# Kernel tuning notes

Hardware: AMD Instinct MI355X
Metric: run time of the kernel (lower is better)

The kernel has to match this reference:

```python
import jax, jax.numpy as jnp
import numpy as np

# dims: batch, dna_seq_len, protein_emb, decoder_size, ffn hidden, vocab, layers, heads
B, T, P, D, F, V, L, H = 64, 128, 1024, 512, 2048, 4096, 4, 8


def _sinusoid_pe(T, D):
    pos = np.arange(T, dtype=np.float32)[:, None]
    div = np.exp(np.arange(0, D, 2, dtype=np.float32) * (-np.log(10000.0) / D))
    pe = np.zeros((T, D), dtype=np.float32)
    pe[:, 0::2] = np.sin(pos * div)
    pe[:, 1::2] = np.cos(pos * div)
    return jnp.asarray(pe)


def setup_inputs() -> dict:
    key = jax.random.key(0)
    ks = iter(jax.random.split(key, 24))
    n = lambda *shape: jax.random.normal(next(ks), shape, jnp.float32) * 0.02
    return dict(
        protein_embeddings=jax.random.normal(next(ks), (B, P), jnp.float32),
        input_token=jax.random.randint(next(ks), (B,), 0, V),
        proj1_w=n(P, 2 * D), proj1_b=jnp.zeros((2 * D,), jnp.float32),
        proj2_w=n(2 * D, D), proj2_b=jnp.zeros((D,), jnp.float32),
        emb=n(V, D),
        sa_w=n(L, 4, D, D), sa_b=jnp.zeros((L, 4, D), jnp.float32),
        ca_w=n(L, 4, D, D), ca_b=jnp.zeros((L, 4, D), jnp.float32),
        ffn_w1=n(L, D, F), ffn_b1=jnp.zeros((L, F), jnp.float32),
        ffn_w2=n(L, F, D), ffn_b2=jnp.zeros((L, D), jnp.float32),
        ln_g=jnp.ones((L, 3, D), jnp.float32), ln_b=jnp.zeros((L, 3, D), jnp.float32),
        out_w=n(D, V), out_b=jnp.zeros((V,), jnp.float32),
        pe=_sinusoid_pe(T, D),
    )


def _layer_norm(x, g, b, eps=1e-5):
    m = jnp.mean(x, -1, keepdims=True)
    v = jnp.var(x, -1, keepdims=True)
    return (x - m) * jax.lax.rsqrt(v + eps) * g + b


def _forward(protein_embeddings, input_token, proj1_w, proj1_b, proj2_w, proj2_b,
             emb, sa_w, sa_b, ca_w, ca_b, ffn_w1, ffn_b1, ffn_w2, ffn_b2,
             ln_g, ln_b, out_w, out_b, pe):
    dh = D // H
    scale = 1.0 / jnp.sqrt(jnp.float32(dh))
    # protein -> decoder memory: Linear(P, 2D) -> ReLU -> Linear(2D, D),
    # then repeated along seq dim (memory rows are all identical).
    h = jax.nn.relu(protein_embeddings @ proj1_w + proj1_b)
    mem1 = h @ proj2_w + proj2_b                         # [B, D]
    mem = jnp.broadcast_to(mem1[:, None, :], (B, T, D))  # [B, T, D]
    # Cross-attn K/V are constant across decode steps: precompute per layer.
    K = (jnp.einsum('btd,lde->lbte', mem, ca_w[:, 1]) + ca_b[:, 1][:, None, None, :]).reshape(L, B, T, H, dh)
    Vv = (jnp.einsum('btd,lde->lbte', mem, ca_w[:, 2]) + ca_b[:, 2][:, None, None, :]).reshape(L, B, T, H, dh)

    def step(token, t):
        # query length == 1 (the module embeds only the current token each step)
        x = emb[token] + pe[t]                           # [B, D]
        for l in range(L):
            # self-attn over a single key: softmax over one score == 1,
            # so attn output reduces to Wo(Wv x + bv) + bo
            sa = (x @ sa_w[l, 2] + sa_b[l, 2]) @ sa_w[l, 3] + sa_b[l, 3]
            x = _layer_norm(x + sa, ln_g[l, 0], ln_b[l, 0])
            # cross-attention over protein memory
            q = ((x @ ca_w[l, 0] + ca_b[l, 0]) * scale).reshape(B, H, dh)
            s = jnp.einsum('bhe,bthe->bht', q, K[l])
            a = jax.nn.softmax(s, -1)
            o = jnp.einsum('bht,bthe->bhe', a, Vv[l]).reshape(B, D)
            ca = o @ ca_w[l, 3] + ca_b[l, 3]
            x = _layer_norm(x + ca, ln_g[l, 1], ln_b[l, 1])
            # FFN (ReLU, post-LN as in PyTorch default TransformerDecoderLayer)
            f = jax.nn.relu(x @ ffn_w1[l] + ffn_b1[l]) @ ffn_w2[l] + ffn_b2[l]
            x = _layer_norm(x + f, ln_g[l, 2], ln_b[l, 2])
        logits = x @ out_w + out_b                       # [B, V]
        probs = jax.nn.softmax(logits, -1)
        return jnp.argmax(probs, -1), probs

    _, probs_t = jax.lax.scan(step, input_token, jnp.arange(T))
    return jnp.transpose(probs_t, (1, 0, 2))             # [B, T, V]


def reference(protein_embeddings, input_token, proj1_w, proj1_b, proj2_w, proj2_b,
              emb, sa_w, sa_b, ca_w, ca_b, ffn_w1, ffn_b1, ffn_w2, ffn_b2,
              ln_g, ln_b, out_w, out_b, pe):
    return _forward(protein_embeddings, input_token, proj1_w, proj1_b, proj2_w, proj2_b,
                    emb, sa_w, sa_b, ca_w, ca_b, ffn_w1, ffn_b1, ffn_w2, ffn_b2,
                    ln_g, ln_b, out_w, out_b, pe)
```

## Files before the change

kernel.cpp:

```cpp
#include <hip/hip_runtime.h>


#define B 64
#define T 128
#define PP 1024
#define D 512
#define F 2048
#define V 4096
#define XP 20

typedef const float* fp;

static __device__ __forceinline__ float wred(float s){
    #pragma unroll
    for (int o = 32; o > 0; o >>= 1) s += __shfl_xor(s, o, 64);
    return s;
}

__global__ __launch_bounds__(256) void k_setup_mem(
    fp prot, fp p1w, fp p1b, fp p2w, fp p2b,
    fp caw, fp cab, float* ca_out)
{
    __shared__ float xp[PP];
    __shared__ float hr[PP];
    __shared__ float m1[D];
    __shared__ float tv[D];
    int b = blockIdx.x, tid = threadIdx.x;
    for (int i = tid; i < PP; i += 256) xp[i] = prot[b*PP + i];
    __syncthreads();
    for (int c = tid; c < 1024; c += 256){
        float acc = p1b[c];
        for (int k = 0; k < PP; k++) acc = fmaf(xp[k], p1w[k*1024 + c], acc);
        hr[c] = fmaxf(acc, 0.f);
    }
    __syncthreads();
    for (int c = tid; c < D; c += 256){
        float acc = p2b[c];
        for (int k = 0; k < 1024; k++) acc = fmaf(hr[k], p2w[k*D + c], acc);
        m1[c] = acc;
    }
    __syncthreads();
    for (int l = 0; l < 4; l++){
        const float* wv = caw + (size_t)(l*4 + 2)*D*D;
        const float* bv = cab + (l*4 + 2)*D;
        for (int c = tid; c < D; c += 256){
            float acc = bv[c];
            for (int k = 0; k < D; k++) acc = fmaf(m1[k], wv[k*D + c], acc);
            tv[c] = acc;
        }
        __syncthreads();
        const float* wo = caw + (size_t)(l*4 + 3)*D*D;
        const float* bo = cab + (l*4 + 3)*D;
        for (int c = tid; c < D; c += 256){
            float acc = bo[c];
            for (int k = 0; k < D; k++) acc = fmaf(tv[k], wo[k*D + c], acc);
            ca_out[(l*B + b)*D + c] = acc;
        }
        __syncthreads();
    }
}

__global__ __launch_bounds__(256) void k_fold_sa(
    fp saw, fp sab, float* wfold, float* bfold)
{
    int l = blockIdx.x >> 6;
    int kb = blockIdx.x & 63;
    int tid = threadIdx.x;
    const float* Wv = saw + (size_t)(l*4 + 2)*D*D;
    const float* Wo = saw + (size_t)(l*4 + 3)*D*D;
    __shared__ float a[8][D];
    for (int i = tid; i < 8*D; i += 256){
        int r = i >> 9, m = i & 511;
        a[r][m] = Wv[(kb*8 + r)*D + m];
    }
    __syncthreads();
    for (int cc = 0; cc < 2; cc++){
        int c = tid + cc*256;
        float acc[8];
        #pragma unroll
        for (int r = 0; r < 8; r++) acc[r] = 0.f;
        for (int m = 0; m < D; m++){
            float w = Wo[m*D + c];
            #pragma unroll
            for (int r = 0; r < 8; r++) acc[r] = fmaf(a[r][m], w, acc[r]);
        }
        #pragma unroll
        for (int r = 0; r < 8; r++){
            int kg = kb*8 + r;
            wfold[((size_t)l*D + kg)*D + c] = acc[r] + (kg == c ? 1.f : 0.f);
        }
    }
    if (kb == 0){
        const float* bv = sab + (l*4 + 2)*D;
        const float* bo = sab + (l*4 + 3)*D;
        for (int c = tid; c < D; c += 256){
            float acc = bo[c];
            for (int m = 0; m < D; m++) acc = fmaf(bv[m], Wo[m*D + c], acc);
            bfold[l*D + c] = acc;
        }
    }
}


static __device__ void pro_emb(float* xt, const int* tok, fp emb, fp pe,
                               int t, int r0, int d0, int tid)
{
    int lane = tid & 63, wid = tid >> 6;
    for (int i = 0; i < 4; i++){
        int rr = wid*4 + i;
        int tk = tok[r0 + rr];
        const float* er = emb + (size_t)tk*D + d0;
        const float* pr = pe + t*D + d0;
        #pragma unroll
        for (int j = 0; j < 4; j++){
            int d = lane + j*64;
            xt[d*XP + rr] = er[d] + pr[d];
        }
    }
}

static __device__ void pro_ln4(float* xt, const float* u3, fp g, fp bb,
                               int r0, int d0, int tid)
{
    int lane = tid & 63, wid = tid >> 6;
    int jb = d0 >> 6;
    for (int i = 0; i < 4; i++){
        int rr = wid*4 + i, r = r0 + rr;
        float e[8]; float s = 0.f, sq = 0.f;
        #pragma unroll
        for (int j = 0; j < 8; j++){
            int d = lane + j*64;
            float v = u3[r*D + d] + u3[B*D + r*D + d]
                    + u3[2*B*D + r*D + d] + u3[3*B*D + r*D + d];
            e[j] = v; s += v; sq += v*v;
        }
        s = wred(s); sq = wred(sq);
        float mu = s*(1.f/D);
        float rs = rsqrtf(sq*(1.f/D) - mu*mu + 1e-5f);
        #pragma unroll
        for (int j = 0; j < 8; j++){
            int d = lane + j*64;
            if (j >= jb && j < jb + 4)
                xt[(d - d0)*XP + rr] = (e[j]-mu)*rs*g[d] + bb[d];
        }
    }
}

static __device__ void pro_ln2(float* xt, float* zc, const float* u1, const float* ca,
                               fp g0, fp b0, fp g1, fp b1,
                               int r0, int d0, int c0, int tid)
{
    int lane = tid & 63, wid = tid >> 6;
    int jb = d0 >> 6, jc = c0 >> 6;
    for (int i = 0; i < 4; i++){
        int rr = wid*4 + i, r = r0 + rr;
        float e[8]; float s = 0.f, sq = 0.f;
        #pragma unroll
        for (int j = 0; j < 8; j++){
            int d = lane + j*64;
            float v = u1[r*D + d] + u1[B*D + r*D + d];
            e[j] = v; s += v; sq += v*v;
        }
        s = wred(s); sq = wred(sq);
        float mu = s*(1.f/D), rs = rsqrtf(sq*(1.f/D) - mu*mu + 1e-5f);
        s = 0.f; sq = 0.f;
        #pragma unroll
        for (int j = 0; j < 8; j++){
            int d = lane + j*64;
            float v = (e[j]-mu)*rs*g0[d] + b0[d] + ca[r*D + d];
            e[j] = v; s += v; sq += v*v;
        }
        s = wred(s); sq = wred(sq);
        mu = s*(1.f/D); rs = rsqrtf(sq*(1.f/D) - mu*mu + 1e-5f);
        #pragma unroll
        for (int j = 0; j < 8; j++){
            int d = lane + j*64;
            float z = (e[j]-mu)*rs*g1[d] + b1[d];
            if (xt && j >= jb && j < jb + 4) xt[(d - d0)*XP + rr] = z;
            if (zc && j == jc) zc[rr*64 + lane] = z;
        }
    }
}


__global__ __launch_bounds__(256) void k_sa(
    const float* wfold, const float* bfold, const float* u3,
    fp lng, fp lnb, const int* tok, fp emb, fp pe,
    float* u1, int l, int t)
{
    __shared__ float xt[256*XP];
    int bx = blockIdx.x;
    int cb = bx & 7, rbg = (bx >> 3) & 3, ks = bx >> 5;
    int tid = threadIdx.x;
    int r0 = rbg*16, d0 = ks*256;
    if (l == 0) pro_emb(xt, tok, emb, pe, t, r0, d0, tid);
    else        pro_ln4(xt, u3, lng + ((l-1)*3+2)*D, lnb + ((l-1)*3+2)*D, r0, d0, tid);
    __syncthreads();
    int lane = tid & 63, rb = tid >> 6;
    int c = cb*64 + lane;
    const float* W = wfold + (size_t)l*D*D + (size_t)d0*D + c;
    float bias = (ks == 0) ? bfold[l*D + c] : 0.f;
    float a0=bias, a1=bias, a2=bias, a3=bias;
    const float* xc = xt + rb*4;
    #pragma unroll 8
    for (int k = 0; k < 256; k++){
        float w = W[(size_t)k*D];
        float4 xv = *(const float4*)(xc + k*XP);
        a0 = fmaf(xv.x, w, a0); a1 = fmaf(xv.y, w, a1);
        a2 = fmaf(xv.z, w, a2); a3 = fmaf(xv.w, w, a3);
    }
    int r = r0 + rb*4;
    float* o = u1 + ks*B*D;
    o[(r+0)*D + c] = a0; o[(r+1)*D + c] = a1;
    o[(r+2)*D + c] = a2; o[(r+3)*D + c] = a3;
}

__global__ __launch_bounds__(256) void k_ffn1(
    const float* u1, const float* ca, fp lng, fp lnb,
    fp w1, fp b1, float* h, int l)
{
    __shared__ float zt[256*XP];
    int bx = blockIdx.x;
    int cb = bx & 31, rbg = (bx >> 5) & 3, ks = bx >> 7;
    int tid = threadIdx.x;
    int r0 = rbg*16, d0 = ks*256;
    pro_ln2(zt, nullptr, u1, ca + l*B*D,
            lng + l*3*D, lnb + l*3*D, lng + (l*3+1)*D, lnb + (l*3+1)*D,
            r0, d0, 0, tid);
    __syncthreads();
    int lane = tid & 63, rb = tid >> 6;
    int c = cb*64 + lane;
    const float* W = w1 + (size_t)l*D*F + (size_t)d0*F + c;
    float bias = (ks == 0) ? b1[l*F + c] : 0.f;
    float a0=bias, a1=bias, a2=bias, a3=bias;
    const float* xc = zt + rb*4;
    #pragma unroll 8
    for (int k = 0; k < 256; k++){
        float w = W[(size_t)k*F];
        float4 xv = *(const float4*)(xc + k*XP);
        a0 = fmaf(xv.x, w, a0); a1 = fmaf(xv.y, w, a1);
        a2 = fmaf(xv.z, w, a2); a3 = fmaf(xv.w, w, a3);
    }
    int r = r0 + rb*4;
    float* o = h + ks*B*F;
    o[(r+0)*F + c] = a0; o[(r+1)*F + c] = a1;
    o[(r+2)*F + c] = a2; o[(r+3)*F + c] = a3;
}

__global__ __launch_bounds__(256) void k_ffn2(
    const float* u1, const float* ca, fp lng, fp lnb,
    const float* h, fp w2, fp b2, float* u3, int l)
{
    __shared__ float ht[512*XP];
    __shared__ float zc[16*64];
    int bx = blockIdx.x;
    int cb = bx & 7, rbg = (bx >> 3) & 3, kh = bx >> 5;
    int tid = threadIdx.x;
    int r0 = rbg*16, c0 = cb*64;
    if (kh == 0)
        pro_ln2(nullptr, zc, u1, ca + l*B*D,
                lng + l*3*D, lnb + l*3*D, lng + (l*3+1)*D, lnb + (l*3+1)*D,
                r0, 0, c0, tid);
    for (int i = tid; i < 16*512; i += 256){
        int rr = i >> 9, kk = i & 511;
        int gi = (r0+rr)*F + kh*512 + kk;
        ht[kk*XP + rr] = fmaxf(h[gi] + h[B*F + gi], 0.f);
    }
    __syncthreads();
    int lane = tid & 63, rb = tid >> 6;
    int c = c0 + lane;
    const float* W = w2 + (size_t)l*F*D + (size_t)kh*512*D + c;
    float a0, a1, a2, a3;
    if (kh == 0){
        float bb = b2[l*D + c];
        a0 = bb + zc[(rb*4+0)*64 + lane];
        a1 = bb + zc[(rb*4+1)*64 + lane];
        a2 = bb + zc[(rb*4+2)*64 + lane];
        a3 = bb + zc[(rb*4+3)*64 + lane];
    } else { a0=a1=a2=a3=0.f; }
    const float* xc = ht + rb*4;
    #pragma unroll 8
    for (int k = 0; k < 512; k++){
        float w = W[(size_t)k*D];
        float4 xv = *(const float4*)(xc + k*XP);
        a0 = fmaf(xv.x, w, a0); a1 = fmaf(xv.y, w, a1);
        a2 = fmaf(xv.z, w, a2); a3 = fmaf(xv.w, w, a3);
    }
    int r = r0 + rb*4;
    float* o = u3 + kh*B*D;
    o[(r+0)*D + c] = a0; o[(r+1)*D + c] = a1;
    o[(r+2)*D + c] = a2; o[(r+3)*D + c] = a3;
}

__global__ __launch_bounds__(256) void k_logits(
    const float* u3, fp lng, fp lnb, fp outw, fp outb, float* lgt)
{
    __shared__ float xt[256*XP];
    int bx = blockIdx.x;
    int cb = bx & 63, rbg = (bx >> 6) & 3, ks = bx >> 8;
    int tid = threadIdx.x;
    int r0 = rbg*16, d0 = ks*256;
    pro_ln4(xt, u3, lng + 11*D, lnb + 11*D, r0, d0, tid);
    __syncthreads();
    int lane = tid & 63, rb = tid >> 6;
    int c = cb*64 + lane;
    const float* W = outw + (size_t)d0*V + c;
    float bias = (ks == 0) ? outb[c] : 0.f;
    float a0=bias, a1=bias, a2=bias, a3=bias;
    const float* xc = xt + rb*4;
    #pragma unroll 8
    for (int k = 0; k < 256; k++){
        float w = W[(size_t)k*V];
        float4 xv = *(const float4*)(xc + k*XP);
        a0 = fmaf(xv.x, w, a0); a1 = fmaf(xv.y, w, a1);
        a2 = fmaf(xv.z, w, a2); a3 = fmaf(xv.w, w, a3);
    }
    int r = r0 + rb*4;
    float* o = lgt + ks*B*V;
    o[(r+0)*V + c] = a0; o[(r+1)*V + c] = a1;
    o[(r+2)*V + c] = a2; o[(r+3)*V + c] = a3;
}

__global__ __launch_bounds__(256) void k_final(
    const float* lgt, float* out, int* tok, int t)
{
    int b = blockIdx.x, tid = threadIdx.x;
    int lane = tid & 63, wid = tid >> 6;
    __shared__ float sm[4]; __shared__ int si[4]; __shared__ float ss[4];
    const float* l0 = lgt + b*V;
    const float* l1 = lgt + B*V + b*V;
    float m = -3.4e38f; int mi = 0;
    for (int i = tid; i < V; i += 256){
        float v = l0[i] + l1[i];
        if (v > m){ m = v; mi = i; }
    }
    #pragma unroll
    for (int o = 32; o > 0; o >>= 1){
        float om = __shfl_xor(m, o, 64);
        int   oi = __shfl_xor(mi, o, 64);
        if (om > m || (om == m && oi < mi)){ m = om; mi = oi; }
    }
    if (lane == 0){ sm[wid] = m; si[wid] = mi; }
    __syncthreads();
    if (tid == 0){
        #pragma unroll
        for (int w = 1; w < 4; w++)
            if (sm[w] > sm[0] || (sm[w] == sm[0] && si[w] < si[0])){ sm[0]=sm[w]; si[0]=si[w]; }
        tok[b] = si[0];
    }
    __syncthreads();
    m = sm[0];
    float s = 0.f;
    for (int i = tid; i < V; i += 256) s += expf(l0[i] + l1[i] - m);
    s = wred(s);
    if (lane == 0) ss[wid] = s;
    __syncthreads();
    float inv = 1.f / (ss[0] + ss[1] + ss[2] + ss[3]);
    float* orow = out + ((size_t)b*T + t)*V;
    for (int i = tid; i < V; i += 256)
        orow[i] = expf(l0[i] + l1[i] - m) * inv;
}

extern "C" void kernel_launch(void* const* d_in, const int* in_sizes, int n_in,
                              void* d_out, int out_size, void* d_ws, size_t ws_size,
                              hipStream_t stream)
{
    fp prot = (fp)d_in[0];
    const int* itok = (const int*)d_in[1];
    fp p1w=(fp)d_in[2], p1b=(fp)d_in[3], p2w=(fp)d_in[4], p2b=(fp)d_in[5];
    fp emb=(fp)d_in[6], saw=(fp)d_in[7], sab=(fp)d_in[8];
    fp caw=(fp)d_in[9], cab=(fp)d_in[10];
    fp w1=(fp)d_in[11], b1=(fp)d_in[12], w2=(fp)d_in[13], b2=(fp)d_in[14];
    fp lng=(fp)d_in[15], lnb=(fp)d_in[16];
    fp outw=(fp)d_in[17], outb=(fp)d_in[18], pe=(fp)d_in[19];

    char* w = (char*)d_ws;
    float* wfold = (float*)w;  w += (size_t)4*D*D*4;
    float* bfold = (float*)w;  w += 4*D*4;
    float* ca_o  = (float*)w;  w += 4*B*D*4;
    float* u1    = (float*)w;  w += 2*B*D*4;
    float* hbuf  = (float*)w;  w += 2*B*F*4;
    float* u3    = (float*)w;  w += 4*B*D*4;
    float* lgt   = (float*)w;  w += 2*B*V*4;
    int*   tok   = (int*)w;    w += 256;

    float* out = (float*)d_out;

    k_setup_mem<<<64, 256, 0, stream>>>(prot, p1w, p1b, p2w, p2b, caw, cab, ca_o);
    k_fold_sa<<<256, 256, 0, stream>>>(saw, sab, wfold, bfold);

    for (int t = 0; t < T; t++){
        const int* tsrc = (t == 0) ? itok : tok;
        for (int l = 0; l < 4; l++){
            k_sa  <<<64,  256, 0, stream>>>(wfold, bfold, u3, lng, lnb, tsrc, emb, pe, u1, l, t);
            k_ffn1<<<256, 256, 0, stream>>>(u1, ca_o, lng, lnb, w1, b1, hbuf, l);
            k_ffn2<<<128, 256, 0, stream>>>(u1, ca_o, lng, lnb, hbuf, w2, b2, u3, l);
        }
        k_logits<<<512, 256, 0, stream>>>(u3, lng, lnb, outw, outb, lgt);
        k_final <<<64,  256, 0, stream>>>(lgt, out, tok, t);
    }
}
```

Baseline: 44.91 ms.

## Fuse whole decode loop into one persistent kernel with group barriers

Replaces the per-step, per-layer launches (about 1800 small kernels) with a single persistent kernel of 256 blocks. The blocks form 8 independent batch-row groups that synchronise through atomic-counter grid barriers. It also precomputes the layer-0 self-attention projection of every vocabulary embedding and every positional row, so layer 0 becomes a lookup. The aim is to remove launch overhead and the split-K partial-sum buffers. In exchange it relies on all blocks being co-resident for the spin barriers, and it does an extra V×D×D precompute whose output is far larger than the per-step layer-0 matmul it replaces.

```diff
diff --git a/kernel.cpp b/kernel.cpp
--- a/kernel.cpp
+++ b/kernel.cpp
@@ -7,7 +7,6 @@
 #define D 512
 #define F 2048
 #define V 4096
-#define XP 20
 
 typedef const float* fp;
 
@@ -70,8 +69,8 @@
     const float* Wo = saw + (size_t)(l*4 + 3)*D*D;
     __shared__ float a[8][D];
     for (int i = tid; i < 8*D; i += 256){
-        int r = i >> 9, m = i & 511;
-        a[r][m] = Wv[(kb*8 + r)*D + m];
+        int r = i >> 9, mm = i & 511;
+        a[r][mm] = Wv[(kb*8 + r)*D + mm];
     }
     __syncthreads();
     for (int cc = 0; cc < 2; cc++){
@@ -79,10 +78,10 @@
         float acc[8];
         #pragma unroll
         for (int r = 0; r < 8; r++) acc[r] = 0.f;
-        for (int m = 0; m < D; m++){
-            float w = Wo[m*D + c];
+        for (int mm = 0; mm < D; mm++){
+            float w = Wo[mm*D + c];
             #pragma unroll
-            for (int r = 0; r < 8; r++) acc[r] = fmaf(a[r][m], w, acc[r]);
+            for (int r = 0; r < 8; r++) acc[r] = fmaf(a[r][mm], w, acc[r]);
         }
         #pragma unroll
         for (int r = 0; r < 8; r++){
@@ -95,270 +94,377 @@
         const float* bo = sab + (l*4 + 3)*D;
         for (int c = tid; c < D; c += 256){
             float acc = bo[c];
-            for (int m = 0; m < D; m++) acc = fmaf(bv[m], Wo[m*D + c], acc);
+            for (int mm = 0; mm < D; mm++) acc = fmaf(bv[mm], Wo[mm*D + c], acc);
             bfold[l*D + c] = acc;
         }
     }
 }
 
-
-static __device__ void pro_emb(float* xt, const int* tok, fp emb, fp pe,
-                               int t, int r0, int d0, int tid)
+__global__ __launch_bounds__(256) void k_e0(fp emb, const float* wf0, float* E0){
+    __shared__ float et[8*512];
+    int v0 = blockIdx.x*8, tid = threadIdx.x;
+    for (int i = tid; i < 1024; i += 256){
+        int r = i >> 7, k4 = (i & 127)*4;
+        *(float4*)(et + r*512 + k4) = *(const float4*)(emb + (size_t)(v0+r)*512 + k4);
+    }
+    __syncthreads();
+    for (int half = 0; half < 2; half++){
+        int c = tid + half*256;
+        float acc[8] = {0,0,0,0,0,0,0,0};
+        #pragma unroll 2
+        for (int k4 = 0; k4 < 512; k4 += 4){
+            float w0 = wf0[(size_t)(k4+0)*512 + c];
+            float w1 = wf0[(size_t)(k4+1)*512 + c];
+            float w2 = wf0[(size_t)(k4+2)*512 + c];
+            float w3 = wf0[(size_t)(k4+3)*512 + c];
+            #pragma unroll
+            for (int r = 0; r < 8; r++){
+                float4 xv = *(const float4*)(et + r*512 + k4);
+                acc[r] = fmaf(xv.x, w0, fmaf(xv.y, w1, fmaf(xv.z, w2, fmaf(xv.w, w3, acc[r]))));
+            }
+        }
+        #pragma unroll
+        for (int r = 0; r < 8; r++) E0[(size_t)(v0+r)*512 + c] = acc[r];
+    }
+}
+
+__global__ __launch_bounds__(256) void k_pew(fp pe, const float* wf0, const float* bfold,
+                                             float* peW){
+    __shared__ float et[8*512];
+    int t0 = blockIdx.x*8, tid = threadIdx.x;
+    for (int i = tid; i < 1024; i += 256){
+        int r = i >> 7, k4 = (i & 127)*4;
+        *(float4*)(et + r*512 + k4) = *(const float4*)(pe + (size_t)(t0+r)*512 + k4);
+    }
+    __syncthreads();
+    for (int half = 0; half < 2; half++){
+        int c = tid + half*256;
+        float acc[8] = {0,0,0,0,0,0,0,0};
+        #pragma unroll 2
+        for (int k4 = 0; k4 < 512; k4 += 4){
+            float w0 = wf0[(size_t)(k4+0)*512 + c];
+            float w1 = wf0[(size_t)(k4+1)*512 + c];
+            float w2 = wf0[(size_t)(k4+2)*512 + c];
+            float w3 = wf0[(size_t)(k4+3)*512 + c];
+            #pragma unroll
+            for (int r = 0; r < 8; r++){
+                float4 xv = *(const float4*)(et + r*512 + k4);
+                acc[r] = fmaf(xv.x, w0, fmaf(xv.y, w1, fmaf(xv.z, w2, fmaf(xv.w, w3, acc[r]))));
+            }
+        }
+        float bb = bfold[c];
+        #pragma unroll
+        for (int r = 0; r < 8; r++) peW[(size_t)(t0+r)*512 + c] = acc[r] + bb;
+    }
+}
+
+
+__global__ __launch_bounds__(256) void k_decode(
+    const float* wfold, const float* bfold, const float* E0, const float* peW,
+    const float* ca_o, fp w1, fp b1, fp w2, fp b2, fp lng, fp lnb,
+    fp outw, fp outb, const int* itok,
+    float* u1buf, float* zbuf, float* hbuf, float* u3buf, float* lgt,
+    int* tok, int* ctrl, float* out)
 {
-    int lane = tid & 63, wid = tid >> 6;
-    for (int i = 0; i < 4; i++){
-        int rr = wid*4 + i;
-        int tk = tok[r0 + rr];
-        const float* er = emb + (size_t)tk*D + d0;
-        const float* pr = pe + t*D + d0;
-        #pragma unroll
-        for (int j = 0; j < 4; j++){
-            int d = lane + j*64;
-            xt[d*XP + rr] = er[d] + pr[d];
-        }
-    }
-}
-
-static __device__ void pro_ln4(float* xt, const float* u3, fp g, fp bb,
-                               int r0, int d0, int tid)
-{
-    int lane = tid & 63, wid = tid >> 6;
-    int jb = d0 >> 6;
-    for (int i = 0; i < 4; i++){
-        int rr = wid*4 + i, r = r0 + rr;
-        float e[8]; float s = 0.f, sq = 0.f;
-        #pragma unroll
-        for (int j = 0; j < 8; j++){
-            int d = lane + j*64;
-            float v = u3[r*D + d] + u3[B*D + r*D + d]
-                    + u3[2*B*D + r*D + d] + u3[3*B*D + r*D + d];
-            e[j] = v; s += v; sq += v*v;
-        }
-        s = wred(s); sq = wred(sq);
-        float mu = s*(1.f/D);
-        float rs = rsqrtf(sq*(1.f/D) - mu*mu + 1e-5f);
-        #pragma unroll
-        for (int j = 0; j < 8; j++){
-            int d = lane + j*64;
-            if (j >= jb && j < jb + 4)
-                xt[(d - d0)*XP + rr] = (e[j]-mu)*rs*g[d] + bb[d];
-        }
-    }
-}
-
-static __device__ void pro_ln2(float* xt, float* zc, const float* u1, const float* ca,
-                               fp g0, fp b0, fp g1, fp b1,
-                               int r0, int d0, int c0, int tid)
-{
-    int lane = tid & 63, wid = tid >> 6;
-    int jb = d0 >> 6, jc = c0 >> 6;
-    for (int i = 0; i < 4; i++){
-        int rr = wid*4 + i, r = r0 + rr;
-        float e[8]; float s = 0.f, sq = 0.f;
-        #pragma unroll
-        for (int j = 0; j < 8; j++){
-            int d = lane + j*64;
-            float v = u1[r*D + d] + u1[B*D + r*D + d];
-            e[j] = v; s += v; sq += v*v;
-        }
-        s = wred(s); sq = wred(sq);
-        float mu = s*(1.f/D), rs = rsqrtf(sq*(1.f/D) - mu*mu + 1e-5f);
-        s = 0.f; sq = 0.f;
-        #pragma unroll
-        for (int j = 0; j < 8; j++){
-            int d = lane + j*64;
-            float v = (e[j]-mu)*rs*g0[d] + b0[d] + ca[r*D + d];
-            e[j] = v; s += v; sq += v*v;
-        }
-        s = wred(s); sq = wred(sq);
-        mu = s*(1.f/D); rs = rsqrtf(sq*(1.f/D) - mu*mu + 1e-5f);
-        #pragma unroll
-        for (int j = 0; j < 8; j++){
-            int d = lane + j*64;
-            float z = (e[j]-mu)*rs*g1[d] + b1[d];
-            if (xt && j >= jb && j < jb + 4) xt[(d - d0)*XP + rr] = z;
-            if (zc && j == jc) zc[rr*64 + lane] = z;
-        }
-    }
-}
-
-
-__global__ __launch_bounds__(256) void k_sa(
-    const float* wfold, const float* bfold, const float* u3,
-    fp lng, fp lnb, const int* tok, fp emb, fp pe,
-    float* u1, int l, int t)
-{
-    __shared__ float xt[256*XP];
-    int bx = blockIdx.x;
-    int cb = bx & 7, rbg = (bx >> 3) & 3, ks = bx >> 5;
-    int tid = threadIdx.x;
-    int r0 = rbg*16, d0 = ks*256;
-    if (l == 0) pro_emb(xt, tok, emb, pe, t, r0, d0, tid);
-    else        pro_ln4(xt, u3, lng + ((l-1)*3+2)*D, lnb + ((l-1)*3+2)*D, r0, d0, tid);
-    __syncthreads();
-    int lane = tid & 63, rb = tid >> 6;
-    int c = cb*64 + lane;
-    const float* W = wfold + (size_t)l*D*D + (size_t)d0*D + c;
-    float bias = (ks == 0) ? bfold[l*D + c] : 0.f;
-    float a0=bias, a1=bias, a2=bias, a3=bias;
-    const float* xc = xt + rb*4;
-    #pragma unroll 8
-    for (int k = 0; k < 256; k++){
-        float w = W[(size_t)k*D];
-        float4 xv = *(const float4*)(xc + k*XP);
-        a0 = fmaf(xv.x, w, a0); a1 = fmaf(xv.y, w, a1);
-        a2 = fmaf(xv.z, w, a2); a3 = fmaf(xv.w, w, a3);
-    }
-    int r = r0 + rb*4;
-    float* o = u1 + ks*B*D;
-    o[(r+0)*D + c] = a0; o[(r+1)*D + c] = a1;
-    o[(r+2)*D + c] = a2; o[(r+3)*D + c] = a3;
-}
-
-__global__ __launch_bounds__(256) void k_ffn1(
-    const float* u1, const float* ca, fp lng, fp lnb,
-    fp w1, fp b1, float* h, int l)
-{
-    __shared__ float zt[256*XP];
-    int bx = blockIdx.x;
-    int cb = bx & 31, rbg = (bx >> 5) & 3, ks = bx >> 7;
-    int tid = threadIdx.x;
-    int r0 = rbg*16, d0 = ks*256;
-    pro_ln2(zt, nullptr, u1, ca + l*B*D,
-            lng + l*3*D, lnb + l*3*D, lng + (l*3+1)*D, lnb + (l*3+1)*D,
-            r0, d0, 0, tid);
-    __syncthreads();
-    int lane = tid & 63, rb = tid >> 6;
-    int c = cb*64 + lane;
-    const float* W = w1 + (size_t)l*D*F + (size_t)d0*F + c;
-    float bias = (ks == 0) ? b1[l*F + c] : 0.f;
-    float a0=bias, a1=bias, a2=bias, a3=bias;
-    const float* xc = zt + rb*4;
-    #pragma unroll 8
-    for (int k = 0; k < 256; k++){
-        float w = W[(size_t)k*F];
-        float4 xv = *(const float4*)(xc + k*XP);
-        a0 = fmaf(xv.x, w, a0); a1 = fmaf(xv.y, w, a1);
-        a2 = fmaf(xv.z, w, a2); a3 = fmaf(xv.w, w, a3);
-    }
-    int r = r0 + rb*4;
-    float* o = h + ks*B*F;
-    o[(r+0)*F + c] = a0; o[(r+1)*F + c] = a1;
-    o[(r+2)*F + c] = a2; o[(r+3)*F + c] = a3;
-}
-
-__global__ __launch_bounds__(256) void k_ffn2(
-    const float* u1, const float* ca, fp lng, fp lnb,
-    const float* h, fp w2, fp b2, float* u3, int l)
-{
-    __shared__ float ht[512*XP];
-    __shared__ float zc[16*64];
-    int bx = blockIdx.x;
-    int cb = bx & 7, rbg = (bx >> 3) & 3, kh = bx >> 5;
-    int tid = threadIdx.x;
-    int r0 = rbg*16, c0 = cb*64;
-    if (kh == 0)
-        pro_ln2(nullptr, zc, u1, ca + l*B*D,
-                lng + l*3*D, lnb + l*3*D, lng + (l*3+1)*D, lnb + (l*3+1)*D,
-                r0, 0, c0, tid);
-    for (int i = tid; i < 16*512; i += 256){
-        int rr = i >> 9, kk = i & 511;
-        int gi = (r0+rr)*F + kh*512 + kk;
-        ht[kk*XP + rr] = fmaxf(h[gi] + h[B*F + gi], 0.f);
-    }
-    __syncthreads();
-    int lane = tid & 63, rb = tid >> 6;
-    int c = c0 + lane;
-    const float* W = w2 + (size_t)l*F*D + (size_t)kh*512*D + c;
-    float a0, a1, a2, a3;
-    if (kh == 0){
-        float bb = b2[l*D + c];
-        a0 = bb + zc[(rb*4+0)*64 + lane];
-        a1 = bb + zc[(rb*4+1)*64 + lane];
-        a2 = bb + zc[(rb*4+2)*64 + lane];
-        a3 = bb + zc[(rb*4+3)*64 + lane];
-    } else { a0=a1=a2=a3=0.f; }
-    const float* xc = ht + rb*4;
-    #pragma unroll 8
-    for (int k = 0; k < 512; k++){
-        float w = W[(size_t)k*D];
-        float4 xv = *(const float4*)(xc + k*XP);
-        a0 = fmaf(xv.x, w, a0); a1 = fmaf(xv.y, w, a1);
-        a2 = fmaf(xv.z, w, a2); a3 = fmaf(xv.w, w, a3);
-    }
-    int r = r0 + rb*4;
-    float* o = u3 + kh*B*D;
-    o[(r+0)*D + c] = a0; o[(r+1)*D + c] = a1;
-    o[(r+2)*D + c] = a2; o[(r+3)*D + c] = a3;
-}
-
-__global__ __launch_bounds__(256) void k_logits(
-    const float* u3, fp lng, fp lnb, fp outw, fp outb, float* lgt)
-{
-    __shared__ float xt[256*XP];
-    int bx = blockIdx.x;
-    int cb = bx & 63, rbg = (bx >> 6) & 3, ks = bx >> 8;
-    int tid = threadIdx.x;
-    int r0 = rbg*16, d0 = ks*256;
-    pro_ln4(xt, u3, lng + 11*D, lnb + 11*D, r0, d0, tid);
-    __syncthreads();
-    int lane = tid & 63, rb = tid >> 6;
-    int c = cb*64 + lane;
-    const float* W = outw + (size_t)d0*V + c;
-    float bias = (ks == 0) ? outb[c] : 0.f;
-    float a0=bias, a1=bias, a2=bias, a3=bias;
-    const float* xc = xt + rb*4;
-    #pragma unroll 8
-    for (int k = 0; k < 256; k++){
-        float w = W[(size_t)k*V];
-        float4 xv = *(const float4*)(xc + k*XP);
-        a0 = fmaf(xv.x, w, a0); a1 = fmaf(xv.y, w, a1);
-        a2 = fmaf(xv.z, w, a2); a3 = fmaf(xv.w, w, a3);
-    }
-    int r = r0 + rb*4;
-    float* o = lgt + ks*B*V;
-    o[(r+0)*V + c] = a0; o[(r+1)*V + c] = a1;
-    o[(r+2)*V + c] = a2; o[(r+3)*V + c] = a3;
-}
-
-__global__ __launch_bounds__(256) void k_final(
-    const float* lgt, float* out, int* tok, int t)
-{
-    int b = blockIdx.x, tid = threadIdx.x;
-    int lane = tid & 63, wid = tid >> 6;
-    __shared__ float sm[4]; __shared__ int si[4]; __shared__ float ss[4];
-    const float* l0 = lgt + b*V;
-    const float* l1 = lgt + B*V + b*V;
-    float m = -3.4e38f; int mi = 0;
-    for (int i = tid; i < V; i += 256){
-        float v = l0[i] + l1[i];
-        if (v > m){ m = v; mi = i; }
-    }
-    #pragma unroll
-    for (int o = 32; o > 0; o >>= 1){
-        float om = __shfl_xor(m, o, 64);
-        int   oi = __shfl_xor(mi, o, 64);
-        if (om > m || (om == m && oi < mi)){ m = om; mi = oi; }
-    }
-    if (lane == 0){ sm[wid] = m; si[wid] = mi; }
-    __syncthreads();
-    if (tid == 0){
-        #pragma unroll
-        for (int w = 1; w < 4; w++)
-            if (sm[w] > sm[0] || (sm[w] == sm[0] && si[w] < si[0])){ sm[0]=sm[w]; si[0]=si[w]; }
-        tok[b] = si[0];
-    }
-    __syncthreads();
-    m = sm[0];
-    float s = 0.f;
-    for (int i = tid; i < V; i += 256) s += expf(l0[i] + l1[i] - m);
-    s = wred(s);
-    if (lane == 0) ss[wid] = s;
-    __syncthreads();
-    float inv = 1.f / (ss[0] + ss[1] + ss[2] + ss[3]);
-    float* orow = out + ((size_t)b*T + t)*V;
-    for (int i = tid; i < V; i += 256)
-        orow[i] = expf(l0[i] + l1[i] - m) * inv;
+    const int g = blockIdx.x & 7, m = blockIdx.x >> 3;
+    const int r0 = g*8;
+    const int tid = threadIdx.x;
+    const int lane = tid & 63, wv = tid >> 6;
+    int* cnt = ctrl + g*64;
+    int* go  = ctrl + g*64 + 16;
+    int bk = 0;
+    __shared__ float lds[18432];
+    float* scratch = lds + 16384;
+
+    #define GBAR() do {                                                          \
+        bk++;                                                                    \
+        __syncthreads();                                                         \
+        if (tid == 0){                                                           \
+            int v_ = __hip_atomic_fetch_add(cnt, 1, __ATOMIC_ACQ_REL,            \
+                                            __HIP_MEMORY_SCOPE_AGENT);           \
+            if ((v_ & 31) == 31)                                                 \
+                __hip_atomic_store(go, bk, __ATOMIC_RELEASE,                     \
+                                   __HIP_MEMORY_SCOPE_AGENT);                    \
+            else                                                                 \
+                while (__hip_atomic_load(go, __ATOMIC_ACQUIRE,                   \
+                                         __HIP_MEMORY_SCOPE_AGENT) < bk)         \
+                    __builtin_amdgcn_s_sleep(1);                                 \
+        }                                                                        \
+        __syncthreads();                                                         \
+    } while (0)
+
+    #pragma unroll 1
+    for (int t = 0; t < T; t++){
+        #pragma unroll 1
+        for (int l = 0; l < 4; l++){
+            if (l > 0){
+                fp gg = lng + ((l-1)*3+2)*D, bb = lnb + ((l-1)*3+2)*D;
+                #pragma unroll 1
+                for (int h = 0; h < 2; h++){
+                    int r = wv*2 + h;
+                    const float* s = u3buf + (size_t)(r0 + r)*D;
+                    float e[8], su = 0.f, sq = 0.f;
+                    #pragma unroll
+                    for (int j = 0; j < 8; j++){
+                        float v = s[lane + j*64];
+                        e[j] = v; su += v; sq += v*v;
+                    }
+                    su = wred(su); sq = wred(sq);
+                    float mu = su*(1.f/D), rs = rsqrtf(sq*(1.f/D) - mu*mu + 1e-5f);
+                    #pragma unroll
+                    for (int j = 0; j < 8; j++){
+                        int d = lane + j*64;
+                        lds[r*512 + d] = (e[j]-mu)*rs*gg[d] + bb[d];
+                    }
+                }
+                __syncthreads();
+                int c = tid & 15, ks = tid >> 4;
+                int col = m*16 + c;
+                const float* W = wfold + (size_t)l*D*D + col;
+                float acc[8] = {0,0,0,0,0,0,0,0};
+                #pragma unroll 2
+                for (int k4 = 0; k4 < 32; k4 += 4){
+                    int kk = ks*32 + k4;
+                    float w0 = W[(size_t)(kk+0)*D];
+                    float w1_ = W[(size_t)(kk+1)*D];
+                    float w2_ = W[(size_t)(kk+2)*D];
+                    float w3_ = W[(size_t)(kk+3)*D];
+                    #pragma unroll
+                    for (int r = 0; r < 8; r++){
+                        float4 xv = *(const float4*)(lds + r*512 + kk);
+                        acc[r] = fmaf(xv.x, w0, fmaf(xv.y, w1_, fmaf(xv.z, w2_, fmaf(xv.w, w3_, acc[r]))));
+                    }
+                }
+                float* sc = scratch + (ks*16 + c)*8;
+                #pragma unroll
+                for (int j = 0; j < 8; j++) sc[j] = acc[j];
+                __syncthreads();
+                if (tid < 128){
+                    int cc = tid >> 3, r = tid & 7;
+                    float s = 0.f;
+                    #pragma unroll
+                    for (int q = 0; q < 16; q++) s += scratch[(q*16 + cc)*8 + r];
+                    int col2 = m*16 + cc;
+                    u1buf[(size_t)(r0+r)*D + col2] = s + bfold[l*D + col2];
+                }
+                GBAR();
+            }
+            {
+                fp g0 = lng + (l*3)*D,   b0 = lnb + (l*3)*D;
+                fp g1 = lng + (l*3+1)*D, b1v = lnb + (l*3+1)*D;
+                const int* ts = (t == 0) ? itok : tok;
+                #pragma unroll 1
+                for (int h = 0; h < 2; h++){
+                    int r = wv*2 + h, rg = r0 + r;
+                    float e[8], su = 0.f, sq = 0.f;
+                    if (l == 0){
+                        int tk = ts[rg];
+                        const float* er = E0 + (size_t)tk*D;
+                        const float* pr = peW + t*D;
+                        #pragma unroll
+                        for (int j = 0; j < 8; j++){
+                            int d = lane + j*64;
+                            float v = er[d] + pr[d];
+                            e[j] = v; su += v; sq += v*v;
+                        }
+                    } else {
+                        const float* s = u1buf + (size_t)rg*D;
+                        #pragma unroll
+                        for (int j = 0; j < 8; j++){
+                            float v = s[lane + j*64];
+                            e[j] = v; su += v; sq += v*v;
+                        }
+                    }
+                    su = wred(su); sq = wred(sq);
+                    float mu = su*(1.f/D), rs = rsqrtf(sq*(1.f/D) - mu*mu + 1e-5f);
+                    const float* car = ca_o + ((size_t)l*B + rg)*D;
+                    su = 0.f; sq = 0.f;
+                    #pragma unroll
+                    for (int j = 0; j < 8; j++){
+                        int d = lane + j*64;
+                        float v = (e[j]-mu)*rs*g0[d] + b0[d] + car[d];
+                        e[j] = v; su += v; sq += v*v;
+                    }
+                    su = wred(su); sq = wred(sq);
+                    float mu2 = su*(1.f/D), rs2 = rsqrtf(sq*(1.f/D) - mu2*mu2 + 1e-5f);
+                    #pragma unroll
+                    for (int j = 0; j < 8; j++){
+                        int d = lane + j*64;
+                        float z = (e[j]-mu2)*rs2*g1[d] + b1v[d];
+                        lds[r*512 + d] = z;
+                        if (m == 0) zbuf[(size_t)rg*D + d] = z;
+                    }
+                }
+                __syncthreads();
+                int c = tid & 63, ks = tid >> 6;
+                int col = m*64 + c;
+                const float* W = w1 + (size_t)l*D*F + col;
+                float acc[8] = {0,0,0,0,0,0,0,0};
+                #pragma unroll 2
+                for (int k4 = 0; k4 < 128; k4 += 4){
+                    int kk = ks*128 + k4;
+                    float w0 = W[(size_t)(kk+0)*F];
+                    float w1_ = W[(size_t)(kk+1)*F];
+                    float w2_ = W[(size_t)(kk+2)*F];
+                    float w3_ = W[(size_t)(kk+3)*F];
+                    #pragma unroll
+                    for (int r = 0; r < 8; r++){
+                        float4 xv = *(const float4*)(lds + r*512 + kk);
+                        acc[r] = fmaf(xv.x, w0, fmaf(xv.y, w1_, fmaf(xv.z, w2_, fmaf(xv.w, w3_, acc[r]))));
+                    }
+                }
+                float* sc = scratch + (ks*64 + c)*8;
+                #pragma unroll
+                for (int j = 0; j < 8; j++) sc[j] = acc[j];
+                __syncthreads();
+                #pragma unroll
+                for (int o = 0; o < 2; o++){
+                    int idx = tid + o*256;
+                    int cc = idx >> 3, r = idx & 7;
+                    float s = 0.f;
+                    #pragma unroll
+                    for (int q = 0; q < 4; q++) s += scratch[(q*64 + cc)*8 + r];
+                    int col2 = m*64 + cc;
+                    s += b1[l*F + col2];
+                    hbuf[(size_t)(r0+r)*F + col2] = fmaxf(s, 0.f);
+                }
+                GBAR();
+            }
+            {
+                for (int i = tid; i < 4096; i += 256){
+                    int r = i >> 9, k4 = (i & 511)*4;
+                    *(float4*)(lds + r*2048 + k4) =
+                        *(const float4*)(hbuf + (size_t)(r0+r)*F + k4);
+                }
+                __syncthreads();
+                int c = tid & 15, ks = tid >> 4;
+                int col = m*16 + c;
+                const float* W = w2 + (size_t)l*F*D + col;
+                float acc[8] = {0,0,0,0,0,0,0,0};
+                #pragma unroll 2
+                for (int k4 = 0; k4 < 128; k4 += 4){
+                    int kk = ks*128 + k4;
+                    float w0 = W[(size_t)(kk+0)*D];
+                    float w1_ = W[(size_t)(kk+1)*D];
+                    float w2_ = W[(size_t)(kk+2)*D];
+                    float w3_ = W[(size_t)(kk+3)*D];
+                    #pragma unroll
+                    for (int r = 0; r < 8; r++){
+                        float4 xv = *(const float4*)(lds + r*2048 + kk);
+                        acc[r] = fmaf(xv.x, w0, fmaf(xv.y, w1_, fmaf(xv.z, w2_, fmaf(xv.w, w3_, acc[r]))));
+                    }
+                }
+                __syncthreads();
+                float* sc = scratch + (ks*16 + c)*8;
+                #pragma unroll
+                for (int j = 0; j < 8; j++) sc[j] = acc[j];
+                __syncthreads();
+                if (tid < 128){
+                    int cc = tid >> 3, r = tid & 7;
+                    float s = 0.f;
+                    #pragma unroll
+                    for (int q = 0; q < 16; q++) s += scratch[(q*16 + cc)*8 + r];
+                    int col2 = m*16 + cc;
+                    u3buf[(size_t)(r0+r)*D + col2] =
+                        s + b2[l*D + col2] + zbuf[(size_t)(r0+r)*D + col2];
+                }
+                GBAR();
+            }
+        }
+        {
+            fp gg = lng + 11*D, bb = lnb + 11*D;
+            #pragma unroll 1
+            for (int h = 0; h < 2; h++){
+                int r = wv*2 + h;
+                const float* s = u3buf + (size_t)(r0 + r)*D;
+                float e[8], su = 0.f, sq = 0.f;
+                #pragma unroll
+                for (int j = 0; j < 8; j++){
+                    float v = s[lane + j*64];
+                    e[j] = v; su += v; sq += v*v;
+                }
+                su = wred(su); sq = wred(sq);
+                float mu = su*(1.f/D), rs = rsqrtf(sq*(1.f/D) - mu*mu + 1e-5f);
+                #pragma unroll
+                for (int j = 0; j < 8; j++){
+                    int d = lane + j*64;
+                    lds[r*512 + d] = (e[j]-mu)*rs*gg[d] + bb[d];
+                }
+            }
+            __syncthreads();
+            int c = tid & 127, ks = tid >> 7;
+            int col = m*128 + c;
+            const float* W = outw + col;
+            float acc[8] = {0,0,0,0,0,0,0,0};
+            #pragma unroll 2
+            for (int k4 = 0; k4 < 256; k4 += 4){
+                int kk = ks*256 + k4;
+                float w0 = W[(size_t)(kk+0)*V];
+                float w1_ = W[(size_t)(kk+1)*V];
+                float w2_ = W[(size_t)(kk+2)*V];
+                float w3_ = W[(size_t)(kk+3)*V];
+                #pragma unroll
+                for (int r = 0; r < 8; r++){
+                    float4 xv = *(const float4*)(lds + r*512 + kk);
+                    acc[r] = fmaf(xv.x, w0, fmaf(xv.y, w1_, fmaf(xv.z, w2_, fmaf(xv.w, w3_, acc[r]))));
+                }
+            }
+            float* sc = scratch + (ks*128 + c)*8;
+            #pragma unroll
+            for (int j = 0; j < 8; j++) sc[j] = acc[j];
+            __syncthreads();
+            #pragma unroll
+            for (int o = 0; o < 4; o++){
+                int idx = tid + o*256;
+                int cc = idx >> 3, r = idx & 7;
+                float s = scratch[cc*8 + r] + scratch[(128 + cc)*8 + r];
+                int col2 = m*128 + cc;
+                lgt[(size_t)(r0+r)*V + col2] = s + outb[col2];
+            }
+            GBAR();
+        }
+        {
+            if (m < 8){
+                int r = r0 + m;
+                const float* lr = lgt + (size_t)r*V;
+                float mx = -3.4e38f; int mi = 0;
+                for (int i = tid; i < V; i += 256){
+                    float v = lr[i];
+                    if (v > mx){ mx = v; mi = i; }
+                }
+                #pragma unroll
+                for (int o = 32; o > 0; o >>= 1){
+                    float om = __shfl_xor(mx, o, 64);
+                    int   oi = __shfl_xor(mi, o, 64);
+                    if (om > mx || (om == mx && oi < mi)){ mx = om; mi = oi; }
+                }
+                float* sm = scratch;
+                int*   si = (int*)(scratch + 8);
+                float* ssum = scratch + 16;
+                if (lane == 0){ sm[wv] = mx; si[wv] = mi; }
+                __syncthreads();
+                if (tid == 0){
+                    float bm = sm[0]; int bi = si[0];
+                    #pragma unroll
+                    for (int q = 1; q < 4; q++)
+                        if (sm[q] > bm || (sm[q] == bm && si[q] < bi)){ bm = sm[q]; bi = si[q]; }
+                    sm[0] = bm; tok[r] = bi;
+                }
+                __syncthreads();
+                mx = sm[0];
+                float s = 0.f;
+                for (int i = tid; i < V; i += 256) s += expf(lr[i] - mx);
+                s = wred(s);
+                if (lane == 0) ssum[wv] = s;
+                __syncthreads();
+                float inv = 1.f/(ssum[0]+ssum[1]+ssum[2]+ssum[3]);
+                float* orow = out + ((size_t)r*T + t)*V;
+                for (int i = tid; i < V; i += 256) orow[i] = expf(lr[i] - mx)*inv;
+            }
+            GBAR();
+        }
+    }
+    #undef GBAR
 }
 
 extern "C" void kernel_launch(void* const* d_in, const int* in_sizes, int n_in,
@@ -377,26 +483,26 @@
     char* w = (char*)d_ws;
     float* wfold = (float*)w;  w += (size_t)4*D*D*4;
     float* bfold = (float*)w;  w += 4*D*4;
-    float* ca_o  = (float*)w;  w += 4*B*D*4;
-    float* u1    = (float*)w;  w += 2*B*D*4;
-    float* hbuf  = (float*)w;  w += 2*B*F*4;
-    float* u3    = (float*)w;  w += 4*B*D*4;
-    float* lgt   = (float*)w;  w += 2*B*V*4;
+    float* ca_o  = (float*)w;  w += (size_t)4*B*D*4;
+    float* E0    = (float*)w;  w += (size_t)V*D*4;
+    float* peW   = (float*)w;  w += (size_t)T*D*4;
+    float* u1buf = (float*)w;  w += (size_t)B*D*4;
+    float* zbuf  = (float*)w;  w += (size_t)B*D*4;
+    float* hbuf  = (float*)w;  w += (size_t)B*F*4;
+    float* u3buf = (float*)w;  w += (size_t)B*D*4;
+    float* lgt   = (float*)w;  w += (size_t)B*V*4;
     int*   tok   = (int*)w;    w += 256;
+    int*   ctrl  = (int*)w;    w += 8*64*4;
 
     float* out = (float*)d_out;
 
+    hipMemsetAsync(ctrl, 0, 8*64*4, stream);
     k_setup_mem<<<64, 256, 0, stream>>>(prot, p1w, p1b, p2w, p2b, caw, cab, ca_o);
     k_fold_sa<<<256, 256, 0, stream>>>(saw, sab, wfold, bfold);
-
-    for (int t = 0; t < T; t++){
-        const int* tsrc = (t == 0) ? itok : tok;
-        for (int l = 0; l < 4; l++){
-            k_sa  <<<64,  256, 0, stream>>>(wfold, bfold, u3, lng, lnb, tsrc, emb, pe, u1, l, t);
-            k_ffn1<<<256, 256, 0, stream>>>(u1, ca_o, lng, lnb, w1, b1, hbuf, l);
-            k_ffn2<<<128, 256, 0, stream>>>(u1, ca_o, lng, lnb, hbuf, w2, b2, u3, l);
-        }
-        k_logits<<<512, 256, 0, stream>>>(u3, lng, lnb, outw, outb, lgt);
-        k_final <<<64,  256, 0, stream>>>(lgt, out, tok, t);
-    }
-}
+    k_e0 <<<512, 256, 0, stream>>>(emb, wfold, E0);
+    k_pew<<<16, 256, 0, stream>>>(pe, wfold, bfold, peW);
+
+    k_decode<<<256, 256, 0, stream>>>(
+        wfold, bfold, E0, peW, ca_o, w1, b1, w2, b2, lng, lnb,
+        outw, outb, itok, u1buf, zbuf, hbuf, u3buf, lgt, tok, ctrl, out);
+}
```

Measured after the change: 58.70 ms. 1.31x slower.
